# Performance work log

Hardware: AMD Instinct MI355X
Metric: run time of the kernel (lower is better)

Reference implementation:

```python
import jax, jax.numpy as jnp
import numpy as np

N = 40000      # nodes
E = 320000     # edges (no self loops in input; layer adds them)
F_IN = 256
H1, C1 = 4, 128   # layer 1: att_type 'gat', concat=True
H2, C2 = 8, 6     # layer 2: att_type 'linear', concat=False (mean over heads)
BN_EPS = 1e-5
NEG_SLOPE = 0.2


def setup_inputs() -> dict:
    key = jax.random.key(0)
    k = jax.random.split(key, 12)
    x = jax.random.normal(k[0], (N, F_IN), dtype=jnp.float32)
    row = jax.random.randint(k[1], (E,), 0, N)
    off = jax.random.randint(k[2], (E,), 1, N)
    col = (row + off) % N  # guarantees no self-loops (remove_self_loops is then a no-op)
    edge_index = jnp.stack([row, col])
    s1 = 1.0 / np.sqrt(F_IN)
    s2 = 1.0 / np.sqrt(H1 * C1)
    return dict(
        x=x,
        edge_index=edge_index,
        bn1_gamma=jnp.ones((F_IN,), jnp.float32),
        bn1_beta=jnp.zeros((F_IN,), jnp.float32),
        bn1_mean=jax.random.normal(k[3], (F_IN,), jnp.float32) * 0.1,
        bn1_var=jax.random.uniform(k[4], (F_IN,), jnp.float32, 0.5, 1.5),
        W1=jax.random.normal(k[5], (F_IN, H1 * C1), jnp.float32) * s1,
        att1=jax.random.normal(k[6], (1, H1, 2 * C1), jnp.float32) * 0.1,
        b1=jnp.zeros((H1 * C1,), jnp.float32),
        bn2_gamma=jnp.ones((H1 * C1,), jnp.float32),
        bn2_beta=jnp.zeros((H1 * C1,), jnp.float32),
        bn2_mean=jax.random.normal(k[7], (H1 * C1,), jnp.float32) * 0.1,
        bn2_var=jax.random.uniform(k[8], (H1 * C1,), jnp.float32, 0.5, 1.5),
        W2=jax.random.normal(k[9], (H1 * C1, H2 * C2), jnp.float32) * s2,
        att2=jax.random.normal(k[10], (1, H2, 2 * C2), jnp.float32) * 0.1,
        b2=jnp.zeros((C2,), jnp.float32),
    )


def _bn_eval(x, gamma, beta, mean, var):
    # BatchNorm1d in eval mode (running statistics)
    return (x - mean) * (gamma / jnp.sqrt(var + BN_EPS)) + beta


def _segment_softmax(alpha, seg, num_segments):
    # stable softmax over edges grouped by destination node
    m = jax.ops.segment_max(alpha, seg, num_segments=num_segments)
    ex = jnp.exp(alpha - m[seg])
    den = jax.ops.segment_sum(ex, seg, num_segments=num_segments)
    return ex / (den[seg] + 1e-16)


def _geo_layer(x, row, col, W, att, bias, heads, out_c, att_type, concat):
    n = x.shape[0]
    h = (x @ W).reshape(n, heads, out_c)  # [N,H,C]
    h_j = h[col]                          # gather source features per edge [E,H,C]
    if att_type == 'gat':
        # (cat([x_i,x_j]) * att).sum(-1) == per-node left/right projections gathered
        a_i = (h * att[:, :, :out_c]).sum(-1)[row]   # [E,H]
        a_j = (h_j * att[:, :, out_c:]).sum(-1)      # [E,H]
        alpha = jax.nn.leaky_relu(a_i + a_j, NEG_SLOPE)
    elif att_type == 'linear':
        al = (h_j * att[:, :, :out_c]).sum(-1)
        ar = (h_j * att[:, :, out_c:]).sum(-1)
        alpha = jnp.tanh(al + ar)
    else:
        raise ValueError(att_type)
    alpha = _segment_softmax(alpha, row, n)          # neighbor softmax
    msg = h_j * alpha[:, :, None]                    # [E,H,C]
    out = jax.ops.segment_sum(msg, row, num_segments=n)  # scatter-add ('sum' agg)
    if concat:
        out = out.reshape(n, heads * out_c)
    else:
        out = out.mean(axis=1)
    return out + bias


def reference(x, edge_index, bn1_gamma, bn1_beta, bn1_mean, bn1_var, W1, att1, b1,
              bn2_gamma, bn2_beta, bn2_mean, bn2_var, W2, att2, b2):
    n = x.shape[0]
    loop = jnp.arange(n, dtype=edge_index.dtype)
    row = jnp.concatenate([edge_index[0], loop])  # add self loops (input has none)
    col = jnp.concatenate([edge_index[1], loop])
    # layer 1: dropout (identity in eval) -> BN -> GeoLayer(gat) -> act 'linear' (identity)
    out = _bn_eval(x, bn1_gamma, bn1_beta, bn1_mean, bn1_var)
    out = _geo_layer(out, row, col, W1, att1, b1, H1, C1, 'gat', True)
    # layer 2: BN -> GeoLayer(linear) -> elu
    out = _bn_eval(out, bn2_gamma, bn2_beta, bn2_mean, bn2_var)
    out = jax.nn.elu(_geo_layer(out, row, col, W2, att2, b2, H2, C2, 'linear', False))
    return jax.nn.log_softmax(out, axis=1)
```

## Files before the change

kernel.cpp:

```cpp
#include <hip/hip_runtime.h>
#include <math.h>

#define NN   40000
#define NP   40064
#define EE   320000
#define ET   (EE + NN)
#define FIN  256
#define D1   512
#define NEG  0.2f
#define CAP  64

typedef unsigned short ushort;
typedef __attribute__((ext_vector_type(8))) short   s16x8;
typedef __attribute__((ext_vector_type(4))) float   f32x4;
typedef __attribute__((ext_vector_type(4))) unsigned short u16x4;

#define GL16(g,s) __builtin_amdgcn_global_load_lds((const __attribute__((address_space(1))) unsigned*)(g), (__attribute__((address_space(3))) unsigned*)(s), 16, 0, 0)

__device__ __forceinline__ float lrelu(float x){ return x > 0.f ? x : NEG*x; }
__device__ __forceinline__ float b2f(ushort u){ return __uint_as_float(((unsigned)u) << 16); }
__device__ __forceinline__ ushort f2bf(float f){
  unsigned u = __float_as_uint(f);
  return (ushort)((u + 0x7fffu + ((u >> 16) & 1u)) >> 16);
}
__device__ __forceinline__ float wsumf(float v){
#pragma unroll
  for (int o = 32; o > 0; o >>= 1) v += __shfl_xor(v, o);
  return v;
}

__global__ __launch_bounds__(1024) void zero_prep_kernel(int* __restrict__ cnt,
                            ushort* __restrict__ PE,
                            const float* __restrict__ g1, const float* __restrict__ be1,
                            const float* __restrict__ mu1, const float* __restrict__ va1,
                            const float* __restrict__ g2, const float* __restrict__ be2,
                            const float* __restrict__ mu2, const float* __restrict__ va2,
                            const float* __restrict__ b1,
                            float* __restrict__ sc1, float* __restrict__ sh1,
                            float* __restrict__ sc2, float* __restrict__ sh2)
{
  int i = blockIdx.x*1024 + threadIdx.x;
  if (i < NN) cnt[i] = 0;
  if (blockIdx.x == 0){
    int t = threadIdx.x;
    if (t < FIN){ float s = g1[t]*rsqrtf(va1[t]+1e-5f); sc1[t]=s; sh1[t]=be1[t]-mu1[t]*s; }
    if (t < D1){ float s = g2[t]*rsqrtf(va2[t]+1e-5f); sc2[t]=s; sh2[t]=be2[t]+(b1[t]-mu2[t])*s; }
    if (t < 64) PE[((size_t)NN << 6) + t] = 0;
  }
}

__global__ __launch_bounds__(256) void prep_all_kernel(
    const int* __restrict__ rows, const int* __restrict__ cols,
    int* __restrict__ cnt, int* __restrict__ cs,
    const float* __restrict__ W1, const float* __restrict__ W2,
    const float* __restrict__ sc1, const float* __restrict__ sh1,
    const float* __restrict__ sc2, const float* __restrict__ sh2,
    const float* __restrict__ att1, const float* __restrict__ att2,
    ushort* __restrict__ K1T, float* __restrict__ k0v,
    float* __restrict__ c2, float* __restrict__ a2s)
{
  int b = blockIdx.x;
  if (b < 1407){
    int e = b*256 + threadIdx.x;
    if (e >= ET) return;
    int r, c;
    if (e < EE){ r = rows[e]; c = cols[e]; } else { r = e - EE; c = r; }
    int slot = atomicAdd(&cnt[r], 1);
    if (slot < CAP) cs[(r << 6) + slot] = c;
    return;
  }
  if (b < 1631){
    __shared__ float wcol[128];
    __shared__ float red[4];
    int t = b - 1407;
    int k = threadIdx.x;
    float val = 0.f;
    if (t < 200){
      int h;
      if (t < 192){
        h = t & 3; int j = t >> 2;
        if (k < 128){ int kk = h*128 + k; wcol[k] = W2[(size_t)kk*48 + j] * sc2[kk]; }
      } else {
        h = (t - 192) & 3; int off = ((t - 192) >= 4) ? 128 : 0;
        if (k < 128) wcol[k] = att1[h*256 + off + k];
      }
      __syncthreads();
      const float* wr = W1 + (size_t)k*D1 + h*128;
#pragma unroll
      for (int kk = 0; kk < 128; kk += 4){
        float4 wv = *(const float4*)(wr + kk);
        float4 cv = *(const float4*)(wcol + kk);
        val += wv.x*cv.x + wv.y*cv.y + wv.z*cv.z + wv.w*cv.w;
      }
      K1T[(size_t)t*FIN + k] = f2bf(val * sc1[k]);
      float part = wsumf(sh1[k] * val);
      if ((k & 63) == 0) red[k >> 6] = part;
      __syncthreads();
      if (k == 0) k0v[t] = red[0] + red[1] + red[2] + red[3];
    } else {
      K1T[(size_t)t*FIN + k] = 0;
      if (k == 0) k0v[t] = 0.f;
    }
    return;
  }
  {
    int bb = b - 1631;
    if (bb == 0 && threadIdx.x < 48){
      int h = threadIdx.x/6, c = threadIdx.x%6;
      a2s[threadIdx.x] = att2[h*12 + c] + att2[h*12 + 6 + c];
    }
    int w = bb*4 + (threadIdx.x >> 6);
    int lane = threadIdx.x & 63;
    if (w >= 48) return;
    float acc = 0.f;
    for (int k = lane; k < D1; k += 64) acc += sh2[k] * W2[(size_t)k*48 + w];
    acc = wsumf(acc);
    if (lane == 0) c2[w] = acc;
  }
}

__global__ __launch_bounds__(256) void gemmG_mfma(const float* __restrict__ X,
                                                  const ushort* __restrict__ K1T,
                                                  const float* __restrict__ k0v,
                                                  ushort* __restrict__ G,
                                                  float* __restrict__ ai,
                                                  float* __restrict__ aj)
{
  __shared__ ushort As[64*64];
  __shared__ ushort Bs[224*64];
  int row0 = blockIdx.x * 64;
  int tid = threadIdx.x, lane = tid & 63, wave = tid >> 6;
  f32x4 acc[13] = {};
  int srow = lane >> 3;
  int scolb = (lane & 7) * 16;
#pragma unroll
  for (int kt = 0; kt < 4; ++kt){
    int k0 = kt*64;
#pragma unroll
    for (int j = 0; j < 2; ++j){
      int c = wave*2 + j;
      int rl = c*8 + srow;
      int rowg = row0 + rl; if (rowg >= NN) rowg = 0;
      int j0 = ((lane & 7) ^ (rl & 7)) * 8;
      const float* src = X + (size_t)rowg*FIN + k0 + j0;
      float4 v0 = *(const float4*)src;
      float4 v1 = *(const float4*)(src + 4);
      s16x8 o;
      o[0]=(short)f2bf(v0.x); o[1]=(short)f2bf(v0.y); o[2]=(short)f2bf(v0.z); o[3]=(short)f2bf(v0.w);
      o[4]=(short)f2bf(v1.x); o[5]=(short)f2bf(v1.y); o[6]=(short)f2bf(v1.z); o[7]=(short)f2bf(v1.w);
      *(s16x8*)((char*)As + c*1024 + lane*16) = o;
    }
#pragma unroll
    for (int j = 0; j < 7; ++j){
      int c = wave*7 + j;
      int row = c*8 + srow;
      int cb = scolb ^ ((row & 7) << 4);
      GL16((const char*)(K1T + (size_t)row*FIN + k0) + cb, (char*)Bs + c*1024);
    }
    __syncthreads();
#pragma unroll
    for (int kk = 0; kk < 2; ++kk){
      int kb = kk*64 + (lane >> 4)*16;
      int arow = wave*16 + (lane & 15);
      s16x8 a = *(const s16x8*)((const char*)As + arow*128 + (kb ^ ((arow & 7) << 4)));
#pragma unroll
      for (int ni = 0; ni < 13; ++ni){
        int row = ni*16 + (lane & 15);
        s16x8 bfrag = *(const s16x8*)((const char*)Bs + row*128 + (kb ^ ((row & 7) << 4)));
        acc[ni] = __builtin_amdgcn_mfma_f32_16x16x32_bf16(a, bfrag, acc[ni], 0, 0, 0);
      }
    }
    __syncthreads();
  }
  int cl = lane & 15;
#pragma unroll
  for (int ni = 0; ni < 12; ++ni){
    int t = ni*16 + cl;
    float kc = k0v[t];
#pragma unroll
    for (int rr = 0; rr < 4; ++rr){
      int row = row0 + wave*16 + (lane >> 4)*4 + rr;
      G[(size_t)row*192 + t] = f2bf(acc[ni][rr] + kc);
    }
  }
  if (cl < 8){
    float kc = k0v[192 + cl];
#pragma unroll
    for (int rr = 0; rr < 4; ++rr){
      int row = row0 + wave*16 + (lane >> 4)*4 + rr;
      float v = acc[12][rr] + kc;
      if (cl < 4) ai[(size_t)row*4 + cl] = v;
      else        aj[(size_t)row*4 + (cl-4)] = v;
    }
  }
}

__global__ __launch_bounds__(256) void aggA_kernel(const ushort* __restrict__ G,
                                                   const float* __restrict__ ai,
                                                   const float* __restrict__ aj,
                                                   const int* __restrict__ cnt,
                                                   const int* __restrict__ cs,
                                                   const float* __restrict__ c2,
                                                   const float* __restrict__ a2s,
                                                   ushort* __restrict__ PE)
{
  __shared__ float wsh[4][2][64][4];
  __shared__ int   csh[4][2][64];
  int lane = threadIdx.x & 63;
  int wave = threadIdx.x >> 6;
  int n0 = blockIdx.x*8 + wave*2;
  int n1 = n0 + 1;
  int deg0 = cnt[n0]; deg0 = deg0 > CAP ? CAP : deg0;
  int deg1 = cnt[n1]; deg1 = deg1 > CAP ? CAP : deg1;
  float4 an0 = *(const float4*)(ai + (size_t)n0*4);
  float4 an1 = *(const float4*)(ai + (size_t)n1*4);
  bool aclane = lane < 48;
  int lidx = aclane ? lane : 0;
  const char* Gb = (const char*)G + (size_t)lidx*8;

  bool a0 = lane < deg0, a1 = lane < deg1;
  int c0 = 0, c1 = 0;
  float e00=0,e01=0,e02=0,e03=0, e10=0,e11=0,e12=0,e13=0;
  if (a0){
    c0 = cs[(n0 << 6) + lane];
    float4 av = *(const float4*)(aj + (size_t)c0*4);
    e00 = __expf(lrelu(an0.x+av.x)); e01 = __expf(lrelu(an0.y+av.y));
    e02 = __expf(lrelu(an0.z+av.z)); e03 = __expf(lrelu(an0.w+av.w));
  }
  if (a1){
    c1 = cs[(n1 << 6) + lane];
    float4 av = *(const float4*)(aj + (size_t)c1*4);
    e10 = __expf(lrelu(an1.x+av.x)); e11 = __expf(lrelu(an1.y+av.y));
    e12 = __expf(lrelu(an1.z+av.z)); e13 = __expf(lrelu(an1.w+av.w));
  }
  float d00 = wsumf(e00)+1e-16f, d01 = wsumf(e01)+1e-16f;
  float d02 = wsumf(e02)+1e-16f, d03 = wsumf(e03)+1e-16f;
  float d10 = wsumf(e10)+1e-16f, d11 = wsumf(e11)+1e-16f;
  float d12 = wsumf(e12)+1e-16f, d13 = wsumf(e13)+1e-16f;
  wsh[wave][0][lane][0]=e00; wsh[wave][0][lane][1]=e01;
  wsh[wave][0][lane][2]=e02; wsh[wave][0][lane][3]=e03;
  wsh[wave][1][lane][0]=e10; wsh[wave][1][lane][1]=e11;
  wsh[wave][1][lane][2]=e12; wsh[wave][1][lane][3]=e13;
  csh[wave][0][lane] = a0 ? c0*384 : 0;
  csh[wave][1][lane] = a1 ? c1*384 : 0;

  float A00=0,A01=0,A02=0,A03=0, A10=0,A11=0,A12=0,A13=0;
  int dm = deg0 > deg1 ? deg0 : deg1;
  for (int e = 0; e < dm; e += 2){
    int o00 = csh[wave][0][e], o01 = csh[wave][0][e+1];
    int o10 = csh[wave][1][e], o11 = csh[wave][1][e+1];
    u16x4 v00 = *(const u16x4*)(Gb + o00);
    u16x4 v01 = *(const u16x4*)(Gb + o01);
    u16x4 v10 = *(const u16x4*)(Gb + o10);
    u16x4 v11 = *(const u16x4*)(Gb + o11);
    float4 w00 = *(const float4*)wsh[wave][0][e];
    float4 w01 = *(const float4*)wsh[wave][0][e+1];
    float4 w10 = *(const float4*)wsh[wave][1][e];
    float4 w11 = *(const float4*)wsh[wave][1][e+1];
    A00 += w00.x*b2f(v00[0]) + w01.x*b2f(v01[0]);
    A01 += w00.y*b2f(v00[1]) + w01.y*b2f(v01[1]);
    A02 += w00.z*b2f(v00[2]) + w01.z*b2f(v01[2]);
    A03 += w00.w*b2f(v00[3]) + w01.w*b2f(v01[3]);
    A10 += w10.x*b2f(v10[0]) + w11.x*b2f(v11[0]);
    A11 += w10.y*b2f(v10[1]) + w11.y*b2f(v11[1]);
    A12 += w10.z*b2f(v10[2]) + w11.z*b2f(v11[2]);
    A13 += w10.w*b2f(v10[3]) + w11.w*b2f(v11[3]);
  }

  float cc2 = aclane ? c2[lidx] : 0.f;
  float aa2 = aclane ? a2s[lidx] : 0.f;
  float h0 = A00/d00 + A01/d01 + A02/d02 + A03/d03 + cc2;
  float h1_ = A10/d10 + A11/d11 + A12/d12 + A13/d13 + cc2;
  float s0 = h0*aa2, s1 = h1_*aa2;
  float t0 = 0.f, t1 = 0.f;
  int base = (lane/6)*6;
#pragma unroll
  for (int i = 0; i < 6; ++i){ t0 += __shfl(s0, base + i); t1 += __shfl(s1, base + i); }
  if (aclane){
    float eh0 = __expf(tanhf(t0));
    float eh1 = __expf(tanhf(t1));
    ushort* pe0 = PE + ((size_t)n0 << 6);
    ushort* pe1 = PE + ((size_t)n1 << 6);
    pe0[lane] = f2bf(eh0*h0);
    pe1[lane] = f2bf(eh1*h1_);
    if ((lane % 6) == 0){ pe0[48 + lane/6] = f2bf(eh0); pe1[48 + lane/6] = f2bf(eh1); }
  }
}

__global__ __launch_bounds__(256) void agg2_kernel(const ushort* __restrict__ PE,
                                                   const int* __restrict__ cnt,
                                                   const int* __restrict__ cs,
                                                   const float* __restrict__ bias2,
                                                   float* __restrict__ out)
{
  __shared__ int csh[4][2][64];
  int lane = threadIdx.x & 63;
  int wave = threadIdx.x >> 6;
  int n0 = blockIdx.x*8 + wave*2;
  int n1 = n0 + 1;
  int deg0 = cnt[n0]; deg0 = deg0 > CAP ? CAP : deg0;
  int deg1 = cnt[n1]; deg1 = deg1 > CAP ? CAP : deg1;
  int lidx = (lane < 56) ? lane : 0;
  const char* PEb = (const char*)PE + (size_t)lidx*2;
  const int ZOFF = NN << 7;
  csh[wave][0][lane] = (lane < deg0) ? (cs[(n0 << 6) + lane] << 7) : ZOFF;
  csh[wave][1][lane] = (lane < deg1) ? (cs[(n1 << 6) + lane] << 7) : ZOFF;
  float acc0 = 0.f, acc1 = 0.f;
  int dm = deg0 > deg1 ? deg0 : deg1;
  for (int e = 0; e < dm; e += 2){
    int o00 = csh[wave][0][e], o01 = csh[wave][0][e+1];
    int o10 = csh[wave][1][e], o11 = csh[wave][1][e+1];
    float v00 = b2f(*(const ushort*)(PEb + o00));
    float v01 = b2f(*(const ushort*)(PEb + o01));
    float v10 = b2f(*(const ushort*)(PEb + o10));
    float v11 = b2f(*(const ushort*)(PEb + o11));
    acc0 += v00 + v01;
    acc1 += v10 + v11;
  }

  int hh = (lane < 48) ? lane/6 : 0;
  float den0 = __shfl(acc0, 48 + hh);
  float den1 = __shfl(acc1, 48 + hh);
  float v0 = acc0 / den0, v1 = acc1 / den1;
  int cc = lane % 6;
  float s0 = 0.f, s1 = 0.f;
#pragma unroll
  for (int qq = 0; qq < 8; ++qq){ s0 += __shfl(v0, cc + 6*qq); s1 += __shfl(v1, cc + 6*qq); }
  float bb = bias2[cc];
  float u0 = s0*(1.f/8.f) + bb;
  float u1 = s1*(1.f/8.f) + bb;
  u0 = u0 > 0.f ? u0 : (__expf(u0) - 1.f);
  u1 = u1 > 0.f ? u1 : (__expf(u1) - 1.f);
  float val0 = (lane < 6) ? u0 : -1e30f;
  float val1 = (lane < 6) ? u1 : -1e30f;
  float mx0 = val0, mx1 = val1;
#pragma unroll
  for (int o = 1; o < 8; o <<= 1){ mx0 = fmaxf(mx0, __shfl_xor(mx0, o)); mx1 = fmaxf(mx1, __shfl_xor(mx1, o)); }
  float ex0 = (lane < 6) ? __expf(val0 - mx0) : 0.f;
  float ex1 = (lane < 6) ? __expf(val1 - mx1) : 0.f;
#pragma unroll
  for (int o = 1; o < 8; o <<= 1){ ex0 += __shfl_xor(ex0, o); ex1 += __shfl_xor(ex1, o); }
  if (lane < 6){
    out[(size_t)n0*6 + lane] = val0 - mx0 - __logf(ex0);
    out[(size_t)n1*6 + lane] = val1 - mx1 - __logf(ex1);
  }
}

extern "C" void kernel_launch(void* const* d_in, const int* in_sizes, int n_in,
                              void* d_out, int out_size, void* d_ws, size_t ws_size,
                              hipStream_t stream)
{
  (void)in_sizes; (void)n_in; (void)out_size; (void)ws_size;
  const float* x   = (const float*)d_in[0];
  const int*   ei  = (const int*)  d_in[1];
  const float* g1  = (const float*)d_in[2];
  const float* be1 = (const float*)d_in[3];
  const float* mu1 = (const float*)d_in[4];
  const float* va1 = (const float*)d_in[5];
  const float* W1  = (const float*)d_in[6];
  const float* at1 = (const float*)d_in[7];
  const float* b1  = (const float*)d_in[8];
  const float* g2  = (const float*)d_in[9];
  const float* be2 = (const float*)d_in[10];
  const float* mu2 = (const float*)d_in[11];
  const float* va2 = (const float*)d_in[12];
  const float* W2  = (const float*)d_in[13];
  const float* at2 = (const float*)d_in[14];
  const float* b2  = (const float*)d_in[15];
  const int* rows = ei;
  const int* cols = ei + EE;
  float* out = (float*)d_out;

  char* p = (char*)d_ws;
  auto carve = [&](size_t bytes)->void*{ void* r = (void*)p; p += (bytes + 255) & ~(size_t)255; return r; };
  ushort* K1T = (ushort*)carve((size_t)224*FIN*2);
  ushort* G   = (ushort*)carve((size_t)NP*192*2);
  ushort* PE  = (ushort*)carve((size_t)(NN+1)*64*2);
  float* k0v  = (float*)carve(224*4);
  float* c2   = (float*)carve(48*4);
  float* a2s  = (float*)carve(48*4);
  float* ai   = (float*)carve((size_t)NP*4*4);
  float* aj   = (float*)carve((size_t)NP*4*4);
  float* sc1  = (float*)carve(FIN*4);
  float* sh1  = (float*)carve(FIN*4);
  float* sc2  = (float*)carve(D1*4);
  float* sh2  = (float*)carve(D1*4);
  int* cnt    = (int*)carve((size_t)NN*4);
  int* cs     = (int*)carve((size_t)NN*CAP*4);

  zero_prep_kernel<<<40, 1024, 0, stream>>>(cnt, PE, g1,be1,mu1,va1,g2,be2,mu2,va2,b1,
                                            sc1,sh1,sc2,sh2);
  prep_all_kernel<<<1643, 256, 0, stream>>>(rows, cols, cnt, cs,
                                            W1, W2, sc1, sh1, sc2, sh2, at1, at2,
                                            K1T, k0v, c2, a2s);
  gemmG_mfma<<<626, 256, 0, stream>>>(x, K1T, k0v, G, ai, aj);
  aggA_kernel<<<NN/8, 256, 0, stream>>>(G, ai, aj, cnt, cs, c2, a2s, PE);
  agg2_kernel<<<NN/8, 256, 0, stream>>>(PE, cnt, cs, b2, out);
}
```

Baseline: 97.71 us.

## Slice projected features into 8 column slabs and split layer-1 aggregation

The GEMM output G is stored as 8 slabs of 32 bf16 columns per node, so each gather touches a smaller contiguous region with better cache locality. The fused aggregation kernel is split into three: a softmax-denominator kernel, a per-slab aggregation kernel launched with 8x the blocks that recomputes edge weights, and a kernel that finishes the linear-attention prep. The intent is to shrink the gather working set and raise parallelism, at the cost of two extra launches, recomputed exponentials and extra intermediate buffers in global memory.

```diff
diff --git a/kernel.cpp b/kernel.cpp
--- a/kernel.cpp
+++ b/kernel.cpp
@@ -14,6 +14,7 @@
 typedef __attribute__((ext_vector_type(8))) short   s16x8;
 typedef __attribute__((ext_vector_type(4))) float   f32x4;
 typedef __attribute__((ext_vector_type(4))) unsigned short u16x4;
+typedef __attribute__((ext_vector_type(2))) unsigned short u16x2;
 
 #define GL16(g,s) __builtin_amdgcn_global_load_lds((const __attribute__((address_space(1))) unsigned*)(g), (__attribute__((address_space(3))) unsigned*)(s), 16, 0, 0)
 
@@ -122,7 +123,7 @@
 __global__ __launch_bounds__(256) void gemmG_mfma(const float* __restrict__ X,
                                                   const ushort* __restrict__ K1T,
                                                   const float* __restrict__ k0v,
-                                                  ushort* __restrict__ G,
+                                                  ushort* __restrict__ Gs,
                                                   float* __restrict__ ai,
                                                   float* __restrict__ aj)
 {
@@ -176,11 +177,13 @@
 #pragma unroll
   for (int ni = 0; ni < 12; ++ni){
     int t = ni*16 + cl;
+    int j = t >> 2, h = t & 3;
+    int s = j / 6, jj = j - s*6;
     float kc = k0v[t];
 #pragma unroll
     for (int rr = 0; rr < 4; ++rr){
       int row = row0 + wave*16 + (lane >> 4)*4 + rr;
-      G[(size_t)row*192 + t] = f2bf(acc[ni][rr] + kc);
+      Gs[((size_t)(s*NP + row))*32 + jj*4 + h] = f2bf(acc[ni][rr] + kc);
     }
   }
   if (cl < 8){
@@ -195,41 +198,29 @@
   }
 }
 
-__global__ __launch_bounds__(256) void aggA_kernel(const ushort* __restrict__ G,
-                                                   const float* __restrict__ ai,
+__global__ __launch_bounds__(256) void dinv_kernel(const float* __restrict__ ai,
                                                    const float* __restrict__ aj,
                                                    const int* __restrict__ cnt,
                                                    const int* __restrict__ cs,
-                                                   const float* __restrict__ c2,
-                                                   const float* __restrict__ a2s,
-                                                   ushort* __restrict__ PE)
-{
-  __shared__ float wsh[4][2][64][4];
-  __shared__ int   csh[4][2][64];
+                                                   float* __restrict__ dinv)
+{
   int lane = threadIdx.x & 63;
   int wave = threadIdx.x >> 6;
-  int n0 = blockIdx.x*8 + wave*2;
-  int n1 = n0 + 1;
+  int n0 = blockIdx.x*8 + wave*2, n1 = n0 + 1;
   int deg0 = cnt[n0]; deg0 = deg0 > CAP ? CAP : deg0;
   int deg1 = cnt[n1]; deg1 = deg1 > CAP ? CAP : deg1;
   float4 an0 = *(const float4*)(ai + (size_t)n0*4);
   float4 an1 = *(const float4*)(ai + (size_t)n1*4);
-  bool aclane = lane < 48;
-  int lidx = aclane ? lane : 0;
-  const char* Gb = (const char*)G + (size_t)lidx*8;
-
-  bool a0 = lane < deg0, a1 = lane < deg1;
-  int c0 = 0, c1 = 0;
   float e00=0,e01=0,e02=0,e03=0, e10=0,e11=0,e12=0,e13=0;
-  if (a0){
-    c0 = cs[(n0 << 6) + lane];
-    float4 av = *(const float4*)(aj + (size_t)c0*4);
+  if (lane < deg0){
+    int c = cs[(n0 << 6) + lane];
+    float4 av = *(const float4*)(aj + (size_t)c*4);
     e00 = __expf(lrelu(an0.x+av.x)); e01 = __expf(lrelu(an0.y+av.y));
     e02 = __expf(lrelu(an0.z+av.z)); e03 = __expf(lrelu(an0.w+av.w));
   }
-  if (a1){
-    c1 = cs[(n1 << 6) + lane];
-    float4 av = *(const float4*)(aj + (size_t)c1*4);
+  if (lane < deg1){
+    int c = cs[(n1 << 6) + lane];
+    float4 av = *(const float4*)(aj + (size_t)c*4);
     e10 = __expf(lrelu(an1.x+av.x)); e11 = __expf(lrelu(an1.y+av.y));
     e12 = __expf(lrelu(an1.z+av.z)); e13 = __expf(lrelu(an1.w+av.w));
   }
@@ -237,40 +228,92 @@
   float d02 = wsumf(e02)+1e-16f, d03 = wsumf(e03)+1e-16f;
   float d10 = wsumf(e10)+1e-16f, d11 = wsumf(e11)+1e-16f;
   float d12 = wsumf(e12)+1e-16f, d13 = wsumf(e13)+1e-16f;
-  wsh[wave][0][lane][0]=e00; wsh[wave][0][lane][1]=e01;
-  wsh[wave][0][lane][2]=e02; wsh[wave][0][lane][3]=e03;
-  wsh[wave][1][lane][0]=e10; wsh[wave][1][lane][1]=e11;
-  wsh[wave][1][lane][2]=e12; wsh[wave][1][lane][3]=e13;
-  csh[wave][0][lane] = a0 ? c0*384 : 0;
-  csh[wave][1][lane] = a1 ? c1*384 : 0;
-
-  float A00=0,A01=0,A02=0,A03=0, A10=0,A11=0,A12=0,A13=0;
+  if (lane == 0){
+    *(float4*)(dinv + (size_t)n0*4) = make_float4(1.f/d00, 1.f/d01, 1.f/d02, 1.f/d03);
+    *(float4*)(dinv + (size_t)n1*4) = make_float4(1.f/d10, 1.f/d11, 1.f/d12, 1.f/d13);
+  }
+}
+
+__global__ __launch_bounds__(256) void aggS_kernel(const ushort* __restrict__ Gs,
+                                                   const float* __restrict__ ai,
+                                                   const float* __restrict__ aj,
+                                                   const float* __restrict__ dinv,
+                                                   const int* __restrict__ cnt,
+                                                   const int* __restrict__ cs,
+                                                   float* __restrict__ h2g)
+{
+  __shared__ int csh[4][2][64];
+  int bid = blockIdx.x;
+  int s = bid & 7;
+  int grp = bid >> 3;
+  int lane = threadIdx.x & 63;
+  int wave = threadIdx.x >> 6;
+  int n0 = grp*8 + wave*2, n1 = n0 + 1;
+  int deg0 = cnt[n0]; deg0 = deg0 > CAP ? CAP : deg0;
+  int deg1 = cnt[n1]; deg1 = deg1 > CAP ? CAP : deg1;
+  csh[wave][0][lane] = (lane < deg0) ? cs[(n0 << 6) + lane] : 0;
+  csh[wave][1][lane] = (lane < deg1) ? cs[(n1 << 6) + lane] : 0;
+  int g = lane >> 4, l = lane & 15;
+  int hp = l & 1;
+  float4 an0 = *(const float4*)(ai + (size_t)n0*4);
+  float4 an1 = *(const float4*)(ai + (size_t)n1*4);
+  float4 dv0 = *(const float4*)(dinv + (size_t)n0*4);
+  float4 dv1 = *(const float4*)(dinv + (size_t)n1*4);
+  float ai0a = hp ? an0.z : an0.x, ai0b = hp ? an0.w : an0.y;
+  float ai1a = hp ? an1.z : an1.x, ai1b = hp ? an1.w : an1.y;
+  float di0a = hp ? dv0.z : dv0.x, di0b = hp ? dv0.w : dv0.y;
+  float di1a = hp ? dv1.z : dv1.x, di1b = hp ? dv1.w : dv1.y;
+  int lidx = (l < 12) ? l : 0;
+  const ushort* Gb = Gs + (size_t)s*NP*32 + lidx*2;
+  const float* ajb = aj + hp*2;
+  float A0a=0.f, A0b=0.f, A1a=0.f, A1b=0.f;
   int dm = deg0 > deg1 ? deg0 : deg1;
-  for (int e = 0; e < dm; e += 2){
-    int o00 = csh[wave][0][e], o01 = csh[wave][0][e+1];
-    int o10 = csh[wave][1][e], o11 = csh[wave][1][e+1];
-    u16x4 v00 = *(const u16x4*)(Gb + o00);
-    u16x4 v01 = *(const u16x4*)(Gb + o01);
-    u16x4 v10 = *(const u16x4*)(Gb + o10);
-    u16x4 v11 = *(const u16x4*)(Gb + o11);
-    float4 w00 = *(const float4*)wsh[wave][0][e];
-    float4 w01 = *(const float4*)wsh[wave][0][e+1];
-    float4 w10 = *(const float4*)wsh[wave][1][e];
-    float4 w11 = *(const float4*)wsh[wave][1][e+1];
-    A00 += w00.x*b2f(v00[0]) + w01.x*b2f(v01[0]);
-    A01 += w00.y*b2f(v00[1]) + w01.y*b2f(v01[1]);
-    A02 += w00.z*b2f(v00[2]) + w01.z*b2f(v01[2]);
-    A03 += w00.w*b2f(v00[3]) + w01.w*b2f(v01[3]);
-    A10 += w10.x*b2f(v10[0]) + w11.x*b2f(v11[0]);
-    A11 += w10.y*b2f(v10[1]) + w11.y*b2f(v11[1]);
-    A12 += w10.z*b2f(v10[2]) + w11.z*b2f(v11[2]);
-    A13 += w10.w*b2f(v10[3]) + w11.w*b2f(v11[3]);
-  }
-
+  for (int e = 0; e < dm; e += 4){
+    int e0 = e + g;
+    int c0 = csh[wave][0][e0];
+    int c1 = csh[wave][1][e0];
+    float2 aj0 = *(const float2*)(ajb + (size_t)c0*4);
+    float2 aj1 = *(const float2*)(ajb + (size_t)c1*4);
+    u16x2 g0 = *(const u16x2*)(Gb + (size_t)c0*32);
+    u16x2 g1 = *(const u16x2*)(Gb + (size_t)c1*32);
+    float w0a = __expf(lrelu(ai0a + aj0.x)) * di0a;
+    float w0b = __expf(lrelu(ai0b + aj0.y)) * di0b;
+    float w1a = __expf(lrelu(ai1a + aj1.x)) * di1a;
+    float w1b = __expf(lrelu(ai1b + aj1.y)) * di1b;
+    bool a0 = e0 < deg0, a1 = e0 < deg1;
+    w0a = a0 ? w0a : 0.f; w0b = a0 ? w0b : 0.f;
+    w1a = a1 ? w1a : 0.f; w1b = a1 ? w1b : 0.f;
+    A0a += w0a * b2f(g0[0]); A0b += w0b * b2f(g0[1]);
+    A1a += w1a * b2f(g1[0]); A1b += w1b * b2f(g1[1]);
+  }
+  A0a += __shfl_xor(A0a, 16); A0a += __shfl_xor(A0a, 32);
+  A0b += __shfl_xor(A0b, 16); A0b += __shfl_xor(A0b, 32);
+  A1a += __shfl_xor(A1a, 16); A1a += __shfl_xor(A1a, 32);
+  A1b += __shfl_xor(A1b, 16); A1b += __shfl_xor(A1b, 32);
+  float p0 = A0a + A0b;
+  float p1 = A1a + A1b;
+  float t0 = p0 + __shfl_xor(p0, 1);
+  float t1 = p1 + __shfl_xor(p1, 1);
+  if (lane < 12 && !(lane & 1)){
+    h2g[(size_t)n0*48 + s*6 + (lane >> 1)] = t0;
+    h2g[(size_t)n1*48 + s*6 + (lane >> 1)] = t1;
+  }
+}
+
+__global__ __launch_bounds__(256) void pe_kernel(const float* __restrict__ h2g,
+                                                 const float* __restrict__ c2,
+                                                 const float* __restrict__ a2s,
+                                                 ushort* __restrict__ PE)
+{
+  int lane = threadIdx.x & 63;
+  int wave = threadIdx.x >> 6;
+  int n0 = blockIdx.x*8 + wave*2, n1 = n0 + 1;
+  bool aclane = lane < 48;
+  int lidx = aclane ? lane : 0;
   float cc2 = aclane ? c2[lidx] : 0.f;
   float aa2 = aclane ? a2s[lidx] : 0.f;
-  float h0 = A00/d00 + A01/d01 + A02/d02 + A03/d03 + cc2;
-  float h1_ = A10/d10 + A11/d11 + A12/d12 + A13/d13 + cc2;
+  float h0 = (aclane ? h2g[(size_t)n0*48 + lidx] : 0.f) + cc2;
+  float h1_ = (aclane ? h2g[(size_t)n1*48 + lidx] : 0.f) + cc2;
   float s0 = h0*aa2, s1 = h1_*aa2;
   float t0 = 0.f, t1 = 0.f;
   int base = (lane/6)*6;
@@ -374,8 +417,10 @@
   char* p = (char*)d_ws;
   auto carve = [&](size_t bytes)->void*{ void* r = (void*)p; p += (bytes + 255) & ~(size_t)255; return r; };
   ushort* K1T = (ushort*)carve((size_t)224*FIN*2);
-  ushort* G   = (ushort*)carve((size_t)NP*192*2);
+  ushort* Gs  = (ushort*)carve((size_t)8*NP*32*2);
   ushort* PE  = (ushort*)carve((size_t)(NN+1)*64*2);
+  float* h2g  = (float*)carve((size_t)NN*48*4);
+  float* dinv = (float*)carve((size_t)NN*4*4);
   float* k0v  = (float*)carve(224*4);
   float* c2   = (float*)carve(48*4);
   float* a2s  = (float*)carve(48*4);
@@ -393,7 +438,9 @@
   prep_all_kernel<<<1643, 256, 0, stream>>>(rows, cols, cnt, cs,
                                             W1, W2, sc1, sh1, sc2, sh2, at1, at2,
                                             K1T, k0v, c2, a2s);
-  gemmG_mfma<<<626, 256, 0, stream>>>(x, K1T, k0v, G, ai, aj);
-  aggA_kernel<<<NN/8, 256, 0, stream>>>(G, ai, aj, cnt, cs, c2, a2s, PE);
+  gemmG_mfma<<<626, 256, 0, stream>>>(x, K1T, k0v, Gs, ai, aj);
+  dinv_kernel<<<NN/8, 256, 0, stream>>>(ai, aj, cnt, cs, dinv);
+  aggS_kernel<<<NN, 256, 0, stream>>>(Gs, ai, aj, dinv, cnt, cs, h2g);
+  pe_kernel<<<NN/8, 256, 0, stream>>>(h2g, c2, a2s, PE);
   agg2_kernel<<<NN/8, 256, 0, stream>>>(PE, cnt, cs, b2, out);
 }
```

Measured after the change: 156.8 us. 1.61x slower.
